# Kernel optimization log

Hardware: AMD Instinct MI355X
Metric: run time of the kernel (lower is better)

## Reference

```python
import jax, jax.numpy as jnp
import numpy as np

NB, NLOC, NALL, NNEI = 1, 4096, 6144, 64
N_EDGE, N_ANGLE, A_SEL = 262144, 409600, 10
N_DIM, E_DIM, A_DIM, AXIS = 128, 64, 32, 4
SEL_REDUCE = 10.0


def _lin_params(key, din, dout):
    k1, k2 = jax.random.split(key)
    W = jax.random.normal(k1, (din, dout), jnp.float32) / np.float32(np.sqrt(din))
    b = jax.random.normal(k2, (dout,), jnp.float32) * 0.01
    return W, b


def setup_inputs():
    key = jax.random.key(0)
    ks = jax.random.split(key, 20)
    inp = {}
    inp["node_ebd_ext"] = jax.random.normal(ks[0], (NB, NALL, N_DIM), jnp.float32)
    inp["edge_ebd"] = jax.random.normal(ks[1], (N_EDGE, E_DIM), jnp.float32)
    inp["h2"] = jax.random.normal(ks[2], (N_EDGE, 3), jnp.float32)
    inp["angle_ebd"] = jax.random.normal(ks[3], (N_ANGLE, A_DIM), jnp.float32)
    inp["nlist"] = jax.random.randint(ks[4], (NB, NLOC, NNEI), 0, NALL)
    inp["nlist_mask"] = jnp.ones((NB, NLOC, NNEI), jnp.bool_)
    inp["sw"] = jax.random.uniform(ks[5], (N_EDGE,), jnp.float32)
    inp["a_nlist"] = jax.random.randint(ks[6], (NB, NLOC, A_SEL), 0, NALL)
    inp["a_nlist_mask"] = jnp.ones((NB, NLOC, A_SEL), jnp.bool_)
    inp["a_sw"] = jax.random.uniform(ks[7], (N_ANGLE,), jnp.float32)
    n2e = jax.random.randint(ks[8], (N_EDGE,), 0, NB * NLOC)
    n_ext2e = jax.random.randint(ks[9], (N_EDGE,), 0, NB * NALL)
    inp["edge_index"] = jnp.stack([n2e, n_ext2e])
    n2a = jax.random.randint(ks[10], (N_ANGLE,), 0, NB * NLOC)
    eij2a = jax.random.randint(ks[11], (N_ANGLE,), 0, N_EDGE)
    eik2a = jax.random.randint(ks[12], (N_ANGLE,), 0, N_EDGE)
    inp["angle_index"] = jnp.stack([n2a, eij2a, eik2a])
    sym_dim = (N_DIM + E_DIM) * AXIS          # 768
    edge_info_dim = 2 * N_DIM + E_DIM         # 320
    angle_dim = A_DIM + N_DIM + 2 * E_DIM     # 288
    inp["W_node_self"], inp["b_node_self"] = _lin_params(ks[13], N_DIM, N_DIM)
    inp["W_node_sym"], inp["b_node_sym"] = _lin_params(ks[14], sym_dim, N_DIM)
    inp["W_node_edge"], inp["b_node_edge"] = _lin_params(ks[15], edge_info_dim, N_DIM)
    inp["W_edge_self"], inp["b_edge_self"] = _lin_params(ks[16], edge_info_dim, E_DIM)
    inp["W_edge_angle1"], inp["b_edge_angle1"] = _lin_params(ks[17], angle_dim, E_DIM)
    inp["W_edge_angle2"], inp["b_edge_angle2"] = _lin_params(ks[18], E_DIM, E_DIM)
    inp["W_angle_self"], inp["b_angle_self"] = _lin_params(ks[19], angle_dim, A_DIM)
    inp["n_res0"] = jnp.full((N_DIM,), 0.1, jnp.float32)
    inp["n_res1"] = jnp.full((N_DIM,), 0.1, jnp.float32)
    inp["n_res2"] = jnp.full((N_DIM,), 0.1, jnp.float32)
    inp["e_res0"] = jnp.full((E_DIM,), 0.1, jnp.float32)
    inp["e_res1"] = jnp.full((E_DIM,), 0.1, jnp.float32)
    inp["a_res0"] = jnp.full((A_DIM,), 0.1, jnp.float32)
    return inp


def reference(node_ebd_ext, edge_ebd, h2, angle_ebd, nlist, nlist_mask, sw,
              a_nlist, a_nlist_mask, a_sw, edge_index, angle_index,
              W_node_self, b_node_self, W_node_sym, b_node_sym,
              W_node_edge, b_node_edge, W_edge_self, b_edge_self,
              W_edge_angle1, b_edge_angle1, W_edge_angle2, b_edge_angle2,
              W_angle_self, b_angle_self,
              n_res0, n_res1, n_res2, e_res0, e_res1, a_res0):
    act = jax.nn.silu
    nb, nloc, nnei = nlist.shape
    n_dim = node_ebd_ext.shape[-1]
    n_edge = h2.shape[0]
    dyn_e_sel = nnei / SEL_REDUCE
    dyn_a_sel = a_nlist.shape[-1] / SEL_REDUCE
    node_ebd = node_ebd_ext[:, :nloc]
    n2e, n_ext2e = edge_index[0], edge_index[1]
    n2a, eij2a, eik2a = angle_index[0], angle_index[1], angle_index[2]
    nei_node_ebd = node_ebd_ext.reshape(-1, n_dim)[n_ext2e]  # [n_edge, n_dim]
    node_self = act(node_ebd @ W_node_self + b_node_self)

    def sym_op(flat_ebd):
        # symmetrization: outer(h2, sw*ebd) scattered to owners, then grrg
        d = flat_ebd.shape[-1]
        w = flat_ebd * sw[:, None]
        h2g2 = jax.ops.segment_sum(
            (h2[:, :, None] * w[:, None, :]).reshape(n_edge, 3 * d),
            n2e, num_segments=nb * nloc)
        h2g2 = h2g2.reshape(nb, nloc, 3, d) * (dyn_e_sel ** -0.5)
        m = h2g2[..., :AXIS]  # [nb, nloc, 3, axis]
        g = jnp.einsum('blxa,blxd->blad', m, h2g2) / 3.0
        return g.reshape(nb, nloc, AXIS * d)

    sym_edge = sym_op(edge_ebd)
    sym_node = sym_op(nei_node_ebd)
    node_sym = act(jnp.concatenate([sym_edge, sym_node], -1) @ W_node_sym + b_node_sym)
    node_i = node_ebd.reshape(-1, n_dim)[n2e]
    edge_info = jnp.concatenate([node_i, nei_node_ebd, edge_ebd], -1)  # [n_edge, 320]
    node_edge_update = act(edge_info @ W_node_edge + b_node_edge) * sw[:, None]
    node_edge_msg = jax.ops.segment_sum(node_edge_update, n2e, num_segments=nb * nloc).reshape(nb, nloc, -1) / dyn_e_sel
    n_updated = node_ebd + n_res0 * node_self + n_res1 * node_sym + n_res2 * node_edge_msg
    edge_self = act(edge_info @ W_edge_self + b_edge_self)
    node_for_angle = node_ebd.reshape(-1, n_dim)[n2a]
    edge_ik = edge_ebd[eik2a]
    edge_ij = edge_ebd[eij2a]
    angle_info = jnp.concatenate([angle_ebd, node_for_angle, edge_ik, edge_ij], -1)  # [n_angle, 288]
    edge_angle = act(angle_info @ W_edge_angle1 + b_edge_angle1)
    reduced = jax.ops.segment_sum(edge_angle * a_sw[:, None], eij2a, num_segments=n_edge) / (dyn_a_sel ** 0.5)
    edge_angle_msg = act(reduced @ W_edge_angle2 + b_edge_angle2)
    e_updated = edge_ebd + e_res0 * edge_self + e_res1 * edge_angle_msg
    angle_self = act(angle_info @ W_angle_self + b_angle_self)
    a_updated = angle_ebd + a_res0 * angle_self
    return (n_updated, e_updated, a_updated)
```

## Files before the change

kernel.cpp:

```cpp
#include <hip/hip_runtime.h>
#include <hip/hip_bf16.h>

#define NLOC_   4096
#define NALL_   6144
#define NEDGE_  262144
#define NANGLE_ 409600

typedef __bf16 bf16x8 __attribute__((ext_vector_type(8)));
typedef float  f32x4  __attribute__((ext_vector_type(4)));
typedef unsigned short u16;

__device__ __forceinline__ float silu_(float x){ return x / (1.0f + __expf(-x)); }

__device__ __forceinline__ u16 f2bu(float f){
    union { float f; unsigned u; } v; v.f = f;
    unsigned r = v.u + 0x7fffu + ((v.u >> 16) & 1u);
    return (u16)(r >> 16);
}
__device__ __forceinline__ float bu2f(u16 b){
    union { unsigned u; float f; } v; v.u = ((unsigned)b) << 16; return v.f;
}
__device__ __forceinline__ void st_bf16x4(u16* dst, float4 v){
    unsigned lo = (unsigned)f2bu(v.x) | ((unsigned)f2bu(v.y) << 16);
    unsigned hi = (unsigned)f2bu(v.z) | ((unsigned)f2bu(v.w) << 16);
    *reinterpret_cast<uint2*>(dst) = make_uint2(lo, hi);
}

__global__ void k_prep(const float* __restrict__ Wne, const float* __restrict__ Wes,
                       const float* __restrict__ W1,  const float* __restrict__ WA,
                       const float* __restrict__ W2,  const float* __restrict__ Wsym,
                       const float* __restrict__ Wns,
                       u16* __restrict__ WTe, u16* __restrict__ WTa, u16* __restrict__ WT2,
                       u16* __restrict__ WsymT, u16* __restrict__ WnsT)
{
    int b = blockIdx.x, t = threadIdx.x;
    if (b < 192) {
        if (t < 320) WTe[b*320 + t] = f2bu(b < 128 ? Wne[t*128 + b] : Wes[t*64 + (b-128)]);
    } else if (b < 288) {
        int n = b - 192;
        if (t < 288) WTa[n*288 + t] = f2bu(n < 64 ? W1[t*64 + n] : WA[t*32 + (n-64)]);
    } else if (b < 352) {
        int n = b - 288;
        if (t < 64)  WT2[n*64 + t] = f2bu(W2[t*64 + n]);
    } else if (b < 480) {
        int n = b - 352;
        if (t < 768) WsymT[n*768 + t] = f2bu(Wsym[t*128 + n]);
    } else {
        int n = b - 480;
        if (t < 128) WnsT[n*128 + t] = f2bu(Wns[t*128 + n]);
    }
}

__global__ void k_cvt(const float* __restrict__ src, u16* __restrict__ dst, int n4)
{
    int i = blockIdx.x * 256 + threadIdx.x;
    int stride = gridDim.x * 256;
    for (; i < n4; i += stride) {
        float4 v = ((const float4*)src)[i];
        st_bf16x4(&dst[(size_t)i*4], v);
    }
}

__global__ __launch_bounds__(256) void k_nconst(
    const u16* __restrict__ NB, const u16* __restrict__ WTe,
    float* __restrict__ nconst)
{
    __shared__ __align__(16) u16 sN[64][136];
    const int tid = threadIdx.x;
    const int e0 = blockIdx.x * 64;
    #pragma unroll
    for (int f = tid; f < 1024; f += 256) {
        int r = f >> 4, c = f & 15;
        *(uint4*)&sN[r][8*c] = ((const uint4*)&NB[(size_t)(e0 + r)*128])[c];
    }
    __syncthreads();

    const int w = tid >> 6, l = tid & 63;
    const int lr = l & 15, hq = l >> 4, lk = hq * 8;

    f32x4 acc[4][3] = {};
    #pragma unroll
    for (int kk = 0; kk < 4; ++kk) {
        bf16x8 a[4], b[3];
        #pragma unroll
        for (int m = 0; m < 4; ++m)
            a[m] = *(const bf16x8*)&sN[16*m + lr][kk*32 + lk];
        #pragma unroll
        for (int nf = 0; nf < 3; ++nf)
            b[nf] = *(const bf16x8*)&WTe[(size_t)(48*w + 16*nf + lr)*320 + kk*32 + lk];
        #pragma unroll
        for (int m = 0; m < 4; ++m)
            #pragma unroll
            for (int nf = 0; nf < 3; ++nf)
                acc[m][nf] = __builtin_amdgcn_mfma_f32_16x16x32_bf16(a[m], b[nf], acc[m][nf], 0, 0, 0);
    }
    #pragma unroll
    for (int nf = 0; nf < 3; ++nf) {
        int c = 48*w + 16*nf + lr;
        #pragma unroll
        for (int m = 0; m < 4; ++m)
            #pragma unroll
            for (int j = 0; j < 4; ++j) {
                int r = 16*m + 4*hq + j;
                nconst[(size_t)(e0 + r)*192 + c] = acc[m][nf][j];
            }
    }
}

__global__ void k_count(const int* __restrict__ key, int* __restrict__ cnt)
{
    int e = blockIdx.x * 256 + threadIdx.x;
    atomicAdd(&cnt[key[e]], 1);
}

__global__ void k_scan(const int* __restrict__ cnt, int* __restrict__ off,
                       int* __restrict__ cursor)
{
    __shared__ int wa[1024];
    int t = threadIdx.x;
    int a0 = cnt[4*t], a1 = cnt[4*t+1], a2 = cnt[4*t+2], a3 = cnt[4*t+3];
    int s1 = a0 + a1, s2 = s1 + a2, s3 = s2 + a3;
    wa[t] = s3;
    __syncthreads();
    for (int d = 1; d < 1024; d <<= 1) {
        int x = wa[t];
        int y = (t >= d) ? wa[t-d] : 0;
        __syncthreads();
        wa[t] = x + y;
        __syncthreads();
    }
    int excl = (t == 0) ? 0 : wa[t-1];
    off[4*t]   = excl;        cursor[4*t]   = excl;
    off[4*t+1] = excl + a0;   cursor[4*t+1] = excl + a0;
    off[4*t+2] = excl + s1;   cursor[4*t+2] = excl + s1;
    off[4*t+3] = excl + s2;   cursor[4*t+3] = excl + s2;
    if (t == 1023) off[4096] = excl + s3;
}

__global__ void k_fill_both(const int* __restrict__ key, int* __restrict__ cursor,
                            int* __restrict__ csr, int* __restrict__ rank)
{
    int e = blockIdx.x * 256 + threadIdx.x;
    int pos = atomicAdd(&cursor[key[e]], 1);
    csr[pos] = e;
    rank[e] = pos;
}

__global__ void k_fill_rank(const int* __restrict__ key, int* __restrict__ cursor,
                            int* __restrict__ rank)
{
    int e = blockIdx.x * 256 + threadIdx.x;
    int pos = atomicAdd(&cursor[key[e]], 1);
    rank[e] = pos;
}

__global__ void k_scan2a(const int* __restrict__ cnt2, int* __restrict__ bsum)
{
    __shared__ int wa[256];
    int b = blockIdx.x, t = threadIdx.x;
    int4 v = ((const int4*)cnt2)[b*256 + t];
    wa[t] = v.x + v.y + v.z + v.w;
    __syncthreads();
    for (int d = 128; d > 0; d >>= 1) {
        if (t < d) wa[t] += wa[t+d];
        __syncthreads();
    }
    if (t == 0) bsum[b] = wa[0];
}

__global__ void k_scan2b(const int* __restrict__ bsum, int* __restrict__ boff)
{
    __shared__ int wa[256];
    int t = threadIdx.x;
    wa[t] = bsum[t];
    __syncthreads();
    for (int d = 1; d < 256; d <<= 1) {
        int x = wa[t];
        int y = (t >= d) ? wa[t-d] : 0;
        __syncthreads();
        wa[t] = x + y;
        __syncthreads();
    }
    boff[t] = (t == 0) ? 0 : wa[t-1];
}

__global__ void k_scan2c(const int* __restrict__ cnt2, const int* __restrict__ boff,
                         int* __restrict__ off2, int* __restrict__ cursor2)
{
    __shared__ int wa[256];
    int b = blockIdx.x, t = threadIdx.x;
    int4 v = ((const int4*)cnt2)[b*256 + t];
    int s1 = v.x, s2 = s1 + v.y, s3 = s2 + v.z, s4 = s3 + v.w;
    wa[t] = s4;
    __syncthreads();
    for (int d = 1; d < 256; d <<= 1) {
        int x = wa[t];
        int y = (t >= d) ? wa[t-d] : 0;
        __syncthreads();
        wa[t] = x + y;
        __syncthreads();
    }
    int base = boff[b] + ((t == 0) ? 0 : wa[t-1]);
    int i = (b*256 + t)*4;
    off2[i]   = base;      cursor2[i]   = base;
    off2[i+1] = base + s1; cursor2[i+1] = base + s1;
    off2[i+2] = base + s2; cursor2[i+2] = base + s2;
    off2[i+3] = base + s3; cursor2[i+3] = base + s3;
    if (b == 255 && t == 255) off2[NEDGE_] = NANGLE_;
}

__global__ __launch_bounds__(256, 4) void k_edge_flat(
    const u16* __restrict__ NB, const u16* __restrict__ EB,
    const float* __restrict__ h2, const float* __restrict__ sw,
    const int* __restrict__ n2e, const int* __restrict__ n_ext2e,
    const int* __restrict__ csr,
    const u16* __restrict__ WTe, const float* __restrict__ nconst,
    const float* __restrict__ bne, const float* __restrict__ bes,
    float* __restrict__ msg,
    float* __restrict__ h2g2_e, float* __restrict__ h2g2_n,
    u16* __restrict__ eselfB)
{
    __shared__ __align__(16) u16 sA[64][200];
    __shared__ float sH[4][576];
    __shared__ int   s_eid[64];
    __shared__ int   s_node[64];
    __shared__ int   s_g[64];
    __shared__ float s_sw[64];
    __shared__ float s_h2[64][3];
    __shared__ int   s_segstart[65];
    __shared__ int   s_nseg;

    const int tid = threadIdx.x;
    const int w  = tid >> 6, l = tid & 63;
    const int lr = l & 15, hq = l >> 4, lk = hq * 8;
    const int base = blockIdx.x * 64;

    if (tid < 64) {
        int e = csr[base + tid];
        s_eid[tid]  = e;
        s_node[tid] = n2e[e];
        s_g[tid]    = n_ext2e[e];
        s_sw[tid]   = sw[e];
        s_h2[tid][0] = h2[e*3];
        s_h2[tid][1] = h2[e*3+1];
        s_h2[tid][2] = h2[e*3+2];
    }
    __syncthreads();

    if (tid < 64) {
        bool flag = (tid == 0) || (s_node[tid] != s_node[tid-1]);
        unsigned long long mask = __ballot(flag);
        if (flag) {
            int sid = __popcll(mask & ((1ull << tid) - 1ull));
            s_segstart[sid] = tid;
        }
        if (tid == 0) {
            int ns = __popcll(mask);
            s_nseg = ns;
            s_segstart[ns] = 64;
        }
    }

    #pragma unroll
    for (int f = tid; f < 1024; f += 256) {
        int r = f >> 4, c = f & 15;
        *(uint4*)&sA[r][8*c] = ((const uint4*)&NB[(size_t)s_g[r]*128])[c];
    }
    #pragma unroll
    for (int f = tid; f < 512; f += 256) {
        int r = f >> 3, c = f & 7;
        *(uint4*)&sA[r][128 + 8*c] = ((const uint4*)&EB[(size_t)s_eid[r]*64])[c];
    }
    __syncthreads();

    float bias[3];
    int   cful[3];
    #pragma unroll
    for (int nf = 0; nf < 3; ++nf) {
        int c = 48*w + 16*nf + lr;
        cful[nf] = c;
        bias[nf] = (c < 128) ? bne[c] : bes[c-128];
    }

    f32x4 acc[4][3] = {};
    #pragma unroll
    for (int kk = 0; kk < 6; ++kk) {
        bf16x8 a[4], b[3];
        #pragma unroll
        for (int m = 0; m < 4; ++m)
            a[m] = *(const bf16x8*)&sA[16*m + lr][kk*32 + lk];
        #pragma unroll
        for (int nf = 0; nf < 3; ++nf)
            b[nf] = *(const bf16x8*)&WTe[(size_t)cful[nf]*320 + 128 + kk*32 + lk];
        #pragma unroll
        for (int m = 0; m < 4; ++m)
            #pragma unroll
            for (int nf = 0; nf < 3; ++nf)
                acc[m][nf] = __builtin_amdgcn_mfma_f32_16x16x32_bf16(a[m], b[nf], acc[m][nf], 0, 0, 0);
    }

    #pragma unroll
    for (int nf = 0; nf < 3; ++nf) {
        int c = cful[nf];
        if (c < 128) {
            #pragma unroll
            for (int m = 0; m < 4; ++m)
                #pragma unroll
                for (int j = 0; j < 4; ++j) {
                    int r = 16*m + 4*hq + j;
                    float ncv = nconst[(size_t)s_node[r]*192 + c];
                    acc[m][nf][j] = silu_(acc[m][nf][j] + ncv + bias[nf]) * s_sw[r];
                }
        } else {
            int c2 = c - 128;
            #pragma unroll
            for (int m = 0; m < 4; ++m)
                #pragma unroll
                for (int j = 0; j < 4; ++j) {
                    int r = 16*m + 4*hq + j;
                    float ncv = nconst[(size_t)s_node[r]*192 + c];
                    eselfB[(size_t)(base + r)*64 + c2] =
                        f2bu(silu_(acc[m][nf][j] + ncv + bias[nf]));
                }
        }
    }

    const int nseg = s_nseg;
    for (int s = 0; s < nseg; ++s) {
        int rs = s_segstart[s], re = s_segstart[s+1];
        int nd = s_node[rs];
        #pragma unroll
        for (int nf = 0; nf < 3; ++nf) {
            if (cful[nf] >= 128) continue;
            float v = 0.f;
            #pragma unroll
            for (int m = 0; m < 4; ++m)
                #pragma unroll
                for (int j = 0; j < 4; ++j) {
                    int r = 16*m + 4*hq + j;
                    v += (r >= rs && r < re) ? acc[m][nf][j] : 0.f;
                }
            v += __shfl_xor(v, 16);
            v += __shfl_xor(v, 32);
            if (hq == 0) atomicAdd(&msg[(size_t)nd*128 + cful[nf]], v);
        }
    }

    for (int s = 0; s < nseg; ++s) {
        int rs = s_segstart[s], re = s_segstart[s+1];
        int nd = s_node[rs];
        int lo = max(16*w, rs), hi = min(16*w + 16, re);
        float hacc[9] = {0.f,0.f,0.f,0.f,0.f,0.f,0.f,0.f,0.f};
        for (int r = lo; r < hi; ++r) {
            float swv = s_sw[r];
            float s0 = s_h2[r][0] * swv;
            float s1 = s_h2[r][1] * swv;
            float s2 = s_h2[r][2] * swv;
            float eb = bu2f(sA[r][128 + l]);
            float n0 = bu2f(sA[r][l]);
            float n1 = bu2f(sA[r][64 + l]);
            hacc[0] = fmaf(s0, eb, hacc[0]);
            hacc[1] = fmaf(s1, eb, hacc[1]);
            hacc[2] = fmaf(s2, eb, hacc[2]);
            hacc[3] = fmaf(s0, n0, hacc[3]);
            hacc[4] = fmaf(s0, n1, hacc[4]);
            hacc[5] = fmaf(s1, n0, hacc[5]);
            hacc[6] = fmaf(s1, n1, hacc[6]);
            hacc[7] = fmaf(s2, n0, hacc[7]);
            hacc[8] = fmaf(s2, n1, hacc[8]);
        }
        #pragma unroll
        for (int q = 0; q < 3; ++q) sH[w][q*64 + l] = hacc[q];
        #pragma unroll
        for (int q = 0; q < 6; ++q) sH[w][192 + q*64 + l] = hacc[3+q];
        __syncthreads();
        for (int i = tid; i < 576; i += 256) {
            float v = sH[0][i] + sH[1][i] + sH[2][i] + sH[3][i];
            if (i < 192) atomicAdd(&h2g2_e[(size_t)nd*192 + i], v);
            else         atomicAdd(&h2g2_n[(size_t)nd*384 + (i - 192)], v);
        }
        __syncthreads();
    }
}

__global__ __launch_bounds__(256) void k_angle_mfma(
    const u16* __restrict__ NB, const u16* __restrict__ EB,
    const u16* __restrict__ AB, const float* __restrict__ a_sw,
    const int* __restrict__ n2a, const int* __restrict__ eij2a,
    const int* __restrict__ eik2a, const int* __restrict__ rank2,
    const u16* __restrict__ WTa,
    const float* __restrict__ b1, const float* __restrict__ bA,
    const float* __restrict__ a_res0,
    u16* __restrict__ ea, float* __restrict__ a_out)
{
    __shared__ __align__(16) u16 sA[32][296];
    __shared__ __align__(16) u16 sEA[32][64];
    __shared__ int s_na[32], s_ij[32], s_ik[32], s_rk[32];
    __shared__ float s_asw[32];
    const int tid = threadIdx.x;
    const int a0 = blockIdx.x * 32;

    if (tid < 32) {
        s_na[tid] = n2a[a0 + tid];
        s_ij[tid] = eij2a[a0 + tid];
        s_ik[tid] = eik2a[a0 + tid];
        s_rk[tid] = rank2[a0 + tid];
        s_asw[tid] = a_sw[a0 + tid];
    }
    __syncthreads();

    if (tid < 128) {
        int r = tid >> 2, c = tid & 3;
        *(uint4*)&sA[r][8*c] = ((const uint4*)&AB[(size_t)(a0 + r)*32])[c];
    }
    #pragma unroll
    for (int f = tid; f < 512; f += 256) {
        int r = f >> 4, c = f & 15;
        *(uint4*)&sA[r][32 + 8*c] = ((const uint4*)&NB[(size_t)s_na[r]*128])[c];
    }
    if (tid < 256) {
        int r = tid >> 3, c = tid & 7;
        *(uint4*)&sA[r][160 + 8*c] = ((const uint4*)&EB[(size_t)s_ik[r]*64])[c];
    }
    {
        int f = tid;
        if (f < 256) {
            int r = f >> 3, c = f & 7;
            *(uint4*)&sA[r][224 + 8*c] = ((const uint4*)&EB[(size_t)s_ij[r]*64])[c];
        }
    }
    __syncthreads();

    const int w = tid >> 6, l = tid & 63;
    const int lr = l & 15, hq = l >> 4, lk = hq * 8;
    const int mrow  = (w & 1) * 16;
    const int nbase = (w >> 1) * 48;

    f32x4 acc[3] = {};
    #pragma unroll
    for (int kk = 0; kk < 9; ++kk) {
        bf16x8 a = *(const bf16x8*)&sA[mrow + lr][kk*32 + lk];
        #pragma unroll
        for (int nf = 0; nf < 3; ++nf) {
            bf16x8 b = *(const bf16x8*)&WTa[(size_t)(nbase + 16*nf + lr)*288 + kk*32 + lk];
            acc[nf] = __builtin_amdgcn_mfma_f32_16x16x32_bf16(a, b, acc[nf], 0, 0, 0);
        }
    }

    #pragma unroll
    for (int nf = 0; nf < 3; ++nf) {
        int c = nbase + 16*nf + lr;
        if (c < 64) {
            float bb = b1[c];
            #pragma unroll
            for (int j = 0; j < 4; ++j) {
                int r = mrow + 4*hq + j;
                sEA[r][c] = f2bu(silu_(acc[nf][j] + bb) * s_asw[r]);
            }
        } else {
            int c2 = c - 64;
            float bb = bA[c2], rr = a_res0[c2];
            #pragma unroll
            for (int j = 0; j < 4; ++j) {
                int r = mrow + 4*hq + j;
                size_t idx = (size_t)(a0 + r)*32 + c2;
                a_out[idx] = bu2f(sA[r][c2]) + rr * silu_(acc[nf][j] + bb);
            }
        }
    }
    __syncthreads();

    if (tid < 256) {
        int r = tid >> 3, c = tid & 7;
        *(uint4*)&ea[(size_t)s_rk[r]*64 + 8*c] = *(const uint4*)&sEA[r][8*c];
    }
}

__global__ __launch_bounds__(256) void k_edgefin_mfma(
    const u16* __restrict__ EB, const u16* __restrict__ eselfB,
    const int* __restrict__ rank_e,
    const u16* __restrict__ ea, const int* __restrict__ off2,
    const u16* __restrict__ WT2,
    const float* __restrict__ b2_, const float* __restrict__ er0,
    const float* __restrict__ er1,
    float* __restrict__ e_out)
{
    __shared__ __align__(16) u16 sR[64][72];
    __shared__ __align__(16) u16 sE[64][72];
    __shared__ __align__(16) u16 sB[64][72];
    __shared__ int s_rk[64];
    const int tid = threadIdx.x;
    const int e0 = blockIdx.x * 64;
    const int w = tid >> 6, l = tid & 63;

    if (tid < 64) s_rk[tid] = rank_e[e0 + tid];
    __syncthreads();

    #pragma unroll
    for (int f = tid; f < 512; f += 256) {
        int r = f >> 3, c = f & 7;
        *(uint4*)&sB[r][8*c] = ((const uint4*)&EB[(size_t)(e0 + r)*64])[c];
        *(uint4*)&sE[r][8*c] = ((const uint4*)&eselfB[(size_t)s_rk[r]*64])[c];
    }

    #pragma unroll
    for (int r16 = 0; r16 < 16; ++r16) {
        int r = w*16 + r16;
        int e = e0 + r;
        float s = 0.f;
        int jb = off2[e], je = off2[e+1];
        for (int j = jb; j < je; ++j)
            s += bu2f(ea[(size_t)j*64 + l]);
        sR[r][l] = f2bu(s);
    }
    __syncthreads();

    const int lr = l & 15, hq = l >> 4, lk = hq * 8;

    f32x4 acc[4] = {};
    #pragma unroll
    for (int kk = 0; kk < 2; ++kk) {
        bf16x8 b = *(const bf16x8*)&WT2[(size_t)(16*w + lr)*64 + kk*32 + lk];
        #pragma unroll
        for (int m = 0; m < 4; ++m) {
            bf16x8 a = *(const bf16x8*)&sR[16*m + lr][kk*32 + lk];
            acc[m] = __builtin_amdgcn_mfma_f32_16x16x32_bf16(a, b, acc[m], 0, 0, 0);
        }
    }
    int c = 16*w + lr;
    float bb = b2_[c], r0 = er0[c], r1 = er1[c];
    #pragma unroll
    for (int m = 0; m < 4; ++m)
        #pragma unroll
        for (int j = 0; j < 4; ++j) {
            int r = 16*m + 4*hq + j;
            size_t idx = (size_t)(e0 + r)*64 + c;
            e_out[idx] = bu2f(sB[r][c]) + r0 * bu2f(sE[r][c])
                       + r1 * silu_(acc[m][j] + bb);
        }
}

__global__ void k_symc(const float* __restrict__ h2g2_e,
                       const float* __restrict__ h2g2_n,
                       u16* __restrict__ symcB)
{
    __shared__ float he[192];
    __shared__ float hn[384];
    int n = blockIdx.x;
    int t = threadIdx.x;
    for (int i = t; i < 192; i += 128) he[i] = h2g2_e[(size_t)n*192 + i];
    for (int i = t; i < 384; i += 128) hn[i] = h2g2_n[(size_t)n*384 + i];
    __syncthreads();
    const float SCALE = 1.0f / (6.4f * 3.0f);
    for (int i = t; i < 768; i += 128) {
        float s;
        if (i < 256) {
            int a = i >> 6, j = i & 63;
            s = he[a]*he[j] + he[64+a]*he[64+j] + he[128+a]*he[128+j];
        } else {
            int i2 = i - 256;
            int a = i2 >> 7, j = i2 & 127;
            s = hn[a]*hn[j] + hn[128+a]*hn[128+j] + hn[256+a]*hn[256+j];
        }
        symcB[(size_t)n*768 + i] = f2bu(s * SCALE);
    }
}

__global__ __launch_bounds__(256) void k_node_mfma(
    const u16* __restrict__ symcB, const u16* __restrict__ NB,
    const float* __restrict__ node_ext, const float* __restrict__ msg,
    const u16* __restrict__ WsymT, const u16* __restrict__ WnsT,
    const float* __restrict__ bns, const float* __restrict__ bsym,
    const float* __restrict__ nr0, const float* __restrict__ nr1,
    const float* __restrict__ nr2,
    float* __restrict__ n_out)
{
    __shared__ __align__(16) u16 sA[32][264];
    const int tid = threadIdx.x;
    const int n0 = blockIdx.x * 32;
    const int w = tid >> 6, l = tid & 63;
    const int lr = l & 15, hq = l >> 4, lk = hq * 8;

    f32x4 accY[2][2] = {};
    f32x4 accS[2][2] = {};

    for (int chunk = 0; chunk < 3; ++chunk) {
        __syncthreads();
        #pragma unroll
        for (int f = tid; f < 1024; f += 256) {
            int r = f >> 5, c = f & 31;
            *(uint4*)&sA[r][8*c] =
                ((const uint4*)&symcB[(size_t)(n0 + r)*768 + chunk*256])[c];
        }
        __syncthreads();
        #pragma unroll
        for (int kk = 0; kk < 8; ++kk) {
            bf16x8 a[2], b[2];
            #pragma unroll
            for (int m = 0; m < 2; ++m)
                a[m] = *(const bf16x8*)&sA[16*m + lr][kk*32 + lk];
            #pragma unroll
            for (int nf = 0; nf < 2; ++nf)
                b[nf] = *(const bf16x8*)&WsymT[(size_t)(32*w + 16*nf + lr)*768
                                               + chunk*256 + kk*32 + lk];
            #pragma unroll
            for (int m = 0; m < 2; ++m)
                #pragma unroll
                for (int nf = 0; nf < 2; ++nf)
                    accY[m][nf] = __builtin_amdgcn_mfma_f32_16x16x32_bf16(a[m], b[nf], accY[m][nf], 0, 0, 0);
        }
    }

    __syncthreads();
    #pragma unroll
    for (int f = tid; f < 512; f += 256) {
        int r = f >> 4, c = f & 15;
        *(uint4*)&sA[r][8*c] = ((const uint4*)&NB[(size_t)(n0 + r)*128])[c];
    }
    __syncthreads();
    #pragma unroll
    for (int kk = 0; kk < 4; ++kk) {
        bf16x8 a[2], b[2];
        #pragma unroll
        for (int m = 0; m < 2; ++m)
            a[m] = *(const bf16x8*)&sA[16*m + lr][kk*32 + lk];
        #pragma unroll
        for (int nf = 0; nf < 2; ++nf)
            b[nf] = *(const bf16x8*)&WnsT[(size_t)(32*w + 16*nf + lr)*128 + kk*32 + lk];
        #pragma unroll
        for (int m = 0; m < 2; ++m)
            #pragma unroll
            for (int nf = 0; nf < 2; ++nf)
                accS[m][nf] = __builtin_amdgcn_mfma_f32_16x16x32_bf16(a[m], b[nf], accS[m][nf], 0, 0, 0);
    }

    #pragma unroll
    for (int nf = 0; nf < 2; ++nf) {
        int c = 32*w + 16*nf + lr;
        float bS = bns[c], bY = bsym[c];
        float r0 = nr0[c], r1 = nr1[c], r2 = nr2[c];
        #pragma unroll
        for (int m = 0; m < 2; ++m)
            #pragma unroll
            for (int j = 0; j < 4; ++j) {
                int r = 16*m + 4*hq + j;
                size_t idx = (size_t)(n0 + r)*128 + c;
                float self_ = silu_(accS[m][nf][j] + bS);
                float sym_  = silu_(accY[m][nf][j] + bY);
                n_out[idx] = node_ext[idx] + r0*self_ + r1*sym_
                           + r2 * msg[idx] * (1.0f / 6.4f);
            }
    }
}

extern "C" void kernel_launch(void* const* d_in, const int* in_sizes, int n_in,
                              void* d_out, int out_size, void* d_ws, size_t ws_size,
                              hipStream_t stream)
{
    const float* node_ext  = (const float*)d_in[0];
    const float* edge_ebd  = (const float*)d_in[1];
    const float* h2        = (const float*)d_in[2];
    const float* angle_ebd = (const float*)d_in[3];
    const float* sw        = (const float*)d_in[6];
    const float* a_sw      = (const float*)d_in[9];
    const int*  edge_index  = (const int*)d_in[10];
    const int*  angle_index = (const int*)d_in[11];
    const int* n2e     = edge_index;
    const int* n_ext2e = edge_index + NEDGE_;
    const int* n2a     = angle_index;
    const int* eij2a   = angle_index + NANGLE_;
    const int* eik2a   = angle_index + 2*NANGLE_;

    const float* Wns  = (const float*)d_in[12];
    const float* bns  = (const float*)d_in[13];
    const float* Wsym = (const float*)d_in[14];
    const float* bsym = (const float*)d_in[15];
    const float* Wne  = (const float*)d_in[16];
    const float* bne  = (const float*)d_in[17];
    const float* Wes  = (const float*)d_in[18];
    const float* bes  = (const float*)d_in[19];
    const float* W1   = (const float*)d_in[20];
    const float* b1   = (const float*)d_in[21];
    const float* W2   = (const float*)d_in[22];
    const float* b2_  = (const float*)d_in[23];
    const float* WA   = (const float*)d_in[24];
    const float* bA   = (const float*)d_in[25];
    const float* nr0  = (const float*)d_in[26];
    const float* nr1  = (const float*)d_in[27];
    const float* nr2  = (const float*)d_in[28];
    const float* er0  = (const float*)d_in[29];
    const float* er1  = (const float*)d_in[30];
    const float* ar0  = (const float*)d_in[31];

    char* wsp = (char*)d_ws;
    u16*   ea      = (u16*)wsp;    wsp += (size_t)NANGLE_ * 64 * 2;
    u16*   EB      = (u16*)wsp;    wsp += (size_t)NEDGE_ * 64 * 2;
    u16*   NB      = (u16*)wsp;    wsp += (size_t)NALL_ * 128 * 2;
    u16*   AB      = (u16*)wsp;    wsp += (size_t)NANGLE_ * 32 * 2;
    u16*   eselfB  = (u16*)wsp;    wsp += (size_t)NEDGE_ * 64 * 2;
    u16*   symcB   = (u16*)wsp;    wsp += (size_t)NLOC_ * 768 * 2;
    int*   cnt     = (int*)wsp;    wsp += 4096 * 4;
    int*   cnt2    = (int*)wsp;    wsp += (size_t)NEDGE_ * 4;
    float* msg     = (float*)wsp;  wsp += (size_t)NLOC_ * 128 * 4;
    float* h2g2_e  = (float*)wsp;  wsp += (size_t)NLOC_ * 192 * 4;
    float* h2g2_n  = (float*)wsp;  wsp += (size_t)NLOC_ * 384 * 4;
    size_t zero_bytes = 4096*4 + (size_t)NEDGE_*4 + (size_t)NLOC_*128*4
                      + (size_t)NLOC_*192*4 + (size_t)NLOC_*384*4;
    int*   off     = (int*)wsp;    wsp += 4104 * 4;
    int*   cursor  = (int*)wsp;    wsp += 4096 * 4;
    int*   csr     = (int*)wsp;    wsp += (size_t)NEDGE_ * 4;
    int*   rank_e  = (int*)wsp;    wsp += (size_t)NEDGE_ * 4;
    int*   off2    = (int*)wsp;    wsp += ((size_t)NEDGE_ + 16) * 4;
    int*   cursor2 = (int*)wsp;    wsp += (size_t)NEDGE_ * 4;
    int*   bsum    = (int*)wsp;    wsp += 256 * 4;
    int*   boff    = (int*)wsp;    wsp += 256 * 4;
    int*   rank2   = (int*)wsp;    wsp += (size_t)NANGLE_ * 4;
    float* nconst  = (float*)wsp;  wsp += (size_t)NLOC_ * 192 * 4;
    u16*   WTe     = (u16*)wsp;    wsp += 192 * 320 * 2;
    u16*   WTa     = (u16*)wsp;    wsp += 96 * 288 * 2;
    u16*   WT2     = (u16*)wsp;    wsp += 64 * 64 * 2;
    u16*   WsymT   = (u16*)wsp;    wsp += 128 * 768 * 2;
    u16*   WnsT    = (u16*)wsp;    wsp += 128 * 128 * 2;

    hipMemsetAsync(cnt, 0, zero_bytes, stream);

    float* n_out = (float*)d_out;
    float* e_out = n_out + (size_t)NLOC_ * 128;
    float* a_out = e_out + (size_t)NEDGE_ * 64;

    k_prep   <<<608, 768, 0, stream>>>(Wne, Wes, W1, WA, W2, Wsym, Wns,
                                       WTe, WTa, WT2, WsymT, WnsT);
    k_cvt    <<<768, 256, 0, stream>>>(node_ext, NB, NALL_*128/4);
    k_cvt    <<<4096, 256, 0, stream>>>(edge_ebd, EB, NEDGE_*64/4);
    k_cvt    <<<4096, 256, 0, stream>>>(angle_ebd, AB, NANGLE_*32/4);
    k_count  <<<NEDGE_/256, 256, 0, stream>>>(n2e, cnt);
    k_scan   <<<1, 1024, 0, stream>>>(cnt, off, cursor);
    k_fill_both <<<NEDGE_/256, 256, 0, stream>>>(n2e, cursor, csr, rank_e);
    k_count  <<<NANGLE_/256, 256, 0, stream>>>(eij2a, cnt2);
    k_scan2a <<<256, 256, 0, stream>>>(cnt2, bsum);
    k_scan2b <<<1, 256, 0, stream>>>(bsum, boff);
    k_scan2c <<<256, 256, 0, stream>>>(cnt2, boff, off2, cursor2);
    k_fill_rank <<<NANGLE_/256, 256, 0, stream>>>(eij2a, cursor2, rank2);

    k_nconst <<<NLOC_/64, 256, 0, stream>>>(NB, WTe, nconst);
    k_edge_flat <<<NEDGE_/64, 256, 0, stream>>>(NB, EB, h2, sw, n2e, n_ext2e, csr,
                                                WTe, nconst, bne, bes,
                                                msg, h2g2_e, h2g2_n, eselfB);
    k_angle_mfma <<<NANGLE_/32, 256, 0, stream>>>(NB, EB, AB, a_sw,
                                                  n2a, eij2a, eik2a, rank2,
                                                  WTa, b1, bA, ar0, ea, a_out);
    k_edgefin_mfma <<<NEDGE_/64, 256, 0, stream>>>(EB, eselfB, rank_e, ea, off2,
                                                   WT2, b2_, er0, er1, e_out);
    k_symc   <<<NLOC_, 128, 0, stream>>>(h2g2_e, h2g2_n, symcB);
    k_node_mfma <<<NLOC_/32, 256, 0, stream>>>(symcB, NB, node_ext, msg,
                                               WsymT, WnsT, bns, bsym,
                                               nr0, nr1, nr2, n_out);
}
```

Before: 454.3 us.

## Merge prep, scan, fill and finish kernels into fewer launches; drop rank_e

The weight transposes, bf16 conversions and both histogram counts move into one multi-role kernel. The first scan, the block sums and nconst share a second launch, and the two CSR fills run in a third. Edge-self outputs are now written at the original edge id instead of the sorted rank, which removes the rank_e array and its indirection in the finish kernel. The symc work is folded into the finish kernel. This cuts launch count and serialization, but it is heterogeneous block dispatch with possible imbalance. Writing eselfO by original edge id makes those stores scattered.

```diff
diff --git a/kernel.cpp b/kernel.cpp
--- a/kernel.cpp
+++ b/kernel.cpp
@@ -26,146 +26,139 @@
     *reinterpret_cast<uint2*>(dst) = make_uint2(lo, hi);
 }
 
-__global__ void k_prep(const float* __restrict__ Wne, const float* __restrict__ Wes,
-                       const float* __restrict__ W1,  const float* __restrict__ WA,
-                       const float* __restrict__ W2,  const float* __restrict__ Wsym,
-                       const float* __restrict__ Wns,
-                       u16* __restrict__ WTe, u16* __restrict__ WTa, u16* __restrict__ WT2,
-                       u16* __restrict__ WsymT, u16* __restrict__ WnsT)
-{
-    int b = blockIdx.x, t = threadIdx.x;
-    if (b < 192) {
-        if (t < 320) WTe[b*320 + t] = f2bu(b < 128 ? Wne[t*128 + b] : Wes[t*64 + (b-128)]);
-    } else if (b < 288) {
-        int n = b - 192;
-        if (t < 288) WTa[n*288 + t] = f2bu(n < 64 ? W1[t*64 + n] : WA[t*32 + (n-64)]);
-    } else if (b < 352) {
-        int n = b - 288;
-        if (t < 64)  WT2[n*64 + t] = f2bu(W2[t*64 + n]);
-    } else if (b < 480) {
-        int n = b - 352;
-        if (t < 768) WsymT[n*768 + t] = f2bu(Wsym[t*128 + n]);
+__global__ __launch_bounds__(256) void k_mega_prep(
+    const float* __restrict__ Wne, const float* __restrict__ Wes,
+    const float* __restrict__ W1,  const float* __restrict__ WA,
+    const float* __restrict__ W2,  const float* __restrict__ Wsym,
+    const float* __restrict__ Wns,
+    const float* __restrict__ node_ext, const float* __restrict__ edge_ebd,
+    const float* __restrict__ angle_ebd,
+    const int* __restrict__ n2e, const int* __restrict__ eij2a,
+    u16* __restrict__ WTe, u16* __restrict__ WTa, u16* __restrict__ WT2,
+    u16* __restrict__ WsymT, u16* __restrict__ WnsT,
+    u16* __restrict__ NB, u16* __restrict__ EB, u16* __restrict__ AB,
+    int* __restrict__ cnt, int* __restrict__ cnt2)
+{
+    const int b = blockIdx.x, tid = threadIdx.x;
+    if (b < 812) {
+        int i = b*256 + tid;
+        if (i < 61440) {
+            int r = i/320, c = i - r*320;
+            WTe[i] = f2bu(r < 128 ? Wne[c*128 + r] : Wes[c*64 + (r-128)]);
+        } else if (i < 89088) {
+            int j = i - 61440; int r = j/288, c = j - r*288;
+            WTa[j] = f2bu(r < 64 ? W1[c*64 + r] : WA[c*32 + (r-64)]);
+        } else if (i < 93184) {
+            int j = i - 89088; int r = j >> 6, c = j & 63;
+            WT2[j] = f2bu(W2[c*64 + r]);
+        } else if (i < 191488) {
+            int j = i - 93184; int r = j/768, c = j - r*768;
+            WsymT[j] = f2bu(Wsym[c*128 + r]);
+        } else {
+            int j = i - 191488; int r = j >> 7, c = j & 127;
+            WnsT[j] = f2bu(Wns[c*128 + r]);
+        }
+    } else if (b < 1580) {
+        int i = (b - 812)*256 + tid;
+        float4 v = ((const float4*)node_ext)[i];
+        st_bf16x4(&NB[(size_t)i*4], v);
+    } else if (b < 3628) {
+        for (int i = (b - 1580)*256 + tid; i < NEDGE_*64/4; i += 2048*256) {
+            float4 v = ((const float4*)edge_ebd)[i];
+            st_bf16x4(&EB[(size_t)i*4], v);
+        }
+    } else if (b < 5676) {
+        for (int i = (b - 3628)*256 + tid; i < NANGLE_*32/4; i += 2048*256) {
+            float4 v = ((const float4*)angle_ebd)[i];
+            st_bf16x4(&AB[(size_t)i*4], v);
+        }
+    } else if (b < 6700) {
+        int e = (b - 5676)*256 + tid;
+        atomicAdd(&cnt[n2e[e]], 1);
     } else {
-        int n = b - 480;
-        if (t < 128) WnsT[n*128 + t] = f2bu(Wns[t*128 + n]);
-    }
-}
-
-__global__ void k_cvt(const float* __restrict__ src, u16* __restrict__ dst, int n4)
-{
-    int i = blockIdx.x * 256 + threadIdx.x;
-    int stride = gridDim.x * 256;
-    for (; i < n4; i += stride) {
-        float4 v = ((const float4*)src)[i];
-        st_bf16x4(&dst[(size_t)i*4], v);
-    }
-}
-
-__global__ __launch_bounds__(256) void k_nconst(
+        int a = (b - 6700)*256 + tid;
+        atomicAdd(&cnt2[eij2a[a]], 1);
+    }
+}
+
+__global__ __launch_bounds__(256) void k_scan_misc(
+    const int* __restrict__ cnt, int* __restrict__ off, int* __restrict__ cursor,
+    const int* __restrict__ cnt2, int* __restrict__ bsum,
     const u16* __restrict__ NB, const u16* __restrict__ WTe,
     float* __restrict__ nconst)
 {
     __shared__ __align__(16) u16 sN[64][136];
-    const int tid = threadIdx.x;
-    const int e0 = blockIdx.x * 64;
-    #pragma unroll
-    for (int f = tid; f < 1024; f += 256) {
-        int r = f >> 4, c = f & 15;
-        *(uint4*)&sN[r][8*c] = ((const uint4*)&NB[(size_t)(e0 + r)*128])[c];
-    }
-    __syncthreads();
-
-    const int w = tid >> 6, l = tid & 63;
-    const int lr = l & 15, hq = l >> 4, lk = hq * 8;
-
-    f32x4 acc[4][3] = {};
-    #pragma unroll
-    for (int kk = 0; kk < 4; ++kk) {
-        bf16x8 a[4], b[3];
-        #pragma unroll
-        for (int m = 0; m < 4; ++m)
-            a[m] = *(const bf16x8*)&sN[16*m + lr][kk*32 + lk];
-        #pragma unroll
-        for (int nf = 0; nf < 3; ++nf)
-            b[nf] = *(const bf16x8*)&WTe[(size_t)(48*w + 16*nf + lr)*320 + kk*32 + lk];
-        #pragma unroll
-        for (int m = 0; m < 4; ++m)
+    int* wa = (int*)&sN[0][0];
+    const int b = blockIdx.x, t = threadIdx.x;
+
+    if (b == 0) {
+        int v[16]; int s = 0;
+        #pragma unroll
+        for (int k = 0; k < 16; ++k) { v[k] = s; s += cnt[16*t + k]; }
+        wa[t] = s;
+        __syncthreads();
+        for (int d = 1; d < 256; d <<= 1) {
+            int x = wa[t];
+            int y = (t >= d) ? wa[t-d] : 0;
+            __syncthreads();
+            wa[t] = x + y;
+            __syncthreads();
+        }
+        int excl = (t == 0) ? 0 : wa[t-1];
+        #pragma unroll
+        for (int k = 0; k < 16; ++k) {
+            off[16*t + k]    = excl + v[k];
+            cursor[16*t + k] = excl + v[k];
+        }
+        if (t == 255) off[4096] = excl + s;
+    } else if (b <= 256) {
+        int bb = b - 1;
+        int4 v = ((const int4*)cnt2)[bb*256 + t];
+        wa[t] = v.x + v.y + v.z + v.w;
+        __syncthreads();
+        for (int d = 128; d > 0; d >>= 1) {
+            if (t < d) wa[t] += wa[t+d];
+            __syncthreads();
+        }
+        if (t == 0) bsum[bb] = wa[0];
+    } else {
+        const int e0 = (b - 257) * 64;
+        #pragma unroll
+        for (int f = t; f < 1024; f += 256) {
+            int r = f >> 4, c = f & 15;
+            *(uint4*)&sN[r][8*c] = ((const uint4*)&NB[(size_t)(e0 + r)*128])[c];
+        }
+        __syncthreads();
+        const int w = t >> 6, l = t & 63;
+        const int lr = l & 15, hq = l >> 4, lk = hq * 8;
+        f32x4 acc[4][3] = {};
+        #pragma unroll
+        for (int kk = 0; kk < 4; ++kk) {
+            bf16x8 a[4], bb[3];
+            #pragma unroll
+            for (int m = 0; m < 4; ++m)
+                a[m] = *(const bf16x8*)&sN[16*m + lr][kk*32 + lk];
             #pragma unroll
             for (int nf = 0; nf < 3; ++nf)
-                acc[m][nf] = __builtin_amdgcn_mfma_f32_16x16x32_bf16(a[m], b[nf], acc[m][nf], 0, 0, 0);
-    }
-    #pragma unroll
-    for (int nf = 0; nf < 3; ++nf) {
-        int c = 48*w + 16*nf + lr;
-        #pragma unroll
-        for (int m = 0; m < 4; ++m)
-            #pragma unroll
-            for (int j = 0; j < 4; ++j) {
-                int r = 16*m + 4*hq + j;
-                nconst[(size_t)(e0 + r)*192 + c] = acc[m][nf][j];
-            }
-    }
-}
-
-__global__ void k_count(const int* __restrict__ key, int* __restrict__ cnt)
-{
-    int e = blockIdx.x * 256 + threadIdx.x;
-    atomicAdd(&cnt[key[e]], 1);
-}
-
-__global__ void k_scan(const int* __restrict__ cnt, int* __restrict__ off,
-                       int* __restrict__ cursor)
-{
-    __shared__ int wa[1024];
-    int t = threadIdx.x;
-    int a0 = cnt[4*t], a1 = cnt[4*t+1], a2 = cnt[4*t+2], a3 = cnt[4*t+3];
-    int s1 = a0 + a1, s2 = s1 + a2, s3 = s2 + a3;
-    wa[t] = s3;
-    __syncthreads();
-    for (int d = 1; d < 1024; d <<= 1) {
-        int x = wa[t];
-        int y = (t >= d) ? wa[t-d] : 0;
-        __syncthreads();
-        wa[t] = x + y;
-        __syncthreads();
-    }
-    int excl = (t == 0) ? 0 : wa[t-1];
-    off[4*t]   = excl;        cursor[4*t]   = excl;
-    off[4*t+1] = excl + a0;   cursor[4*t+1] = excl + a0;
-    off[4*t+2] = excl + s1;   cursor[4*t+2] = excl + s1;
-    off[4*t+3] = excl + s2;   cursor[4*t+3] = excl + s2;
-    if (t == 1023) off[4096] = excl + s3;
-}
-
-__global__ void k_fill_both(const int* __restrict__ key, int* __restrict__ cursor,
-                            int* __restrict__ csr, int* __restrict__ rank)
-{
-    int e = blockIdx.x * 256 + threadIdx.x;
-    int pos = atomicAdd(&cursor[key[e]], 1);
-    csr[pos] = e;
-    rank[e] = pos;
-}
-
-__global__ void k_fill_rank(const int* __restrict__ key, int* __restrict__ cursor,
-                            int* __restrict__ rank)
-{
-    int e = blockIdx.x * 256 + threadIdx.x;
-    int pos = atomicAdd(&cursor[key[e]], 1);
-    rank[e] = pos;
-}
-
-__global__ void k_scan2a(const int* __restrict__ cnt2, int* __restrict__ bsum)
-{
-    __shared__ int wa[256];
-    int b = blockIdx.x, t = threadIdx.x;
-    int4 v = ((const int4*)cnt2)[b*256 + t];
-    wa[t] = v.x + v.y + v.z + v.w;
-    __syncthreads();
-    for (int d = 128; d > 0; d >>= 1) {
-        if (t < d) wa[t] += wa[t+d];
-        __syncthreads();
-    }
-    if (t == 0) bsum[b] = wa[0];
+                bb[nf] = *(const bf16x8*)&WTe[(size_t)(48*w + 16*nf + lr)*320 + kk*32 + lk];
+            #pragma unroll
+            for (int m = 0; m < 4; ++m)
+                #pragma unroll
+                for (int nf = 0; nf < 3; ++nf)
+                    acc[m][nf] = __builtin_amdgcn_mfma_f32_16x16x32_bf16(a[m], bb[nf], acc[m][nf], 0, 0, 0);
+        }
+        #pragma unroll
+        for (int nf = 0; nf < 3; ++nf) {
+            int c = 48*w + 16*nf + lr;
+            #pragma unroll
+            for (int m = 0; m < 4; ++m)
+                #pragma unroll
+                for (int j = 0; j < 4; ++j) {
+                    int r = 16*m + 4*hq + j;
+                    nconst[(size_t)(e0 + r)*192 + c] = acc[m][nf][j];
+                }
+        }
+    }
 }
 
 __global__ void k_scan2b(const int* __restrict__ bsum, int* __restrict__ boff)
@@ -207,6 +200,23 @@
     off2[i+2] = base + s2; cursor2[i+2] = base + s2;
     off2[i+3] = base + s3; cursor2[i+3] = base + s3;
     if (b == 255 && t == 255) off2[NEDGE_] = NANGLE_;
+}
+
+__global__ void k_fill2(const int* __restrict__ n2e, int* __restrict__ cursor,
+                        int* __restrict__ csr,
+                        const int* __restrict__ eij2a, int* __restrict__ cursor2,
+                        int* __restrict__ rank2)
+{
+    int b = blockIdx.x;
+    if (b < 1024) {
+        int e = b*256 + threadIdx.x;
+        int pos = atomicAdd(&cursor[n2e[e]], 1);
+        csr[pos] = e;
+    } else {
+        int a = (b - 1024)*256 + threadIdx.x;
+        int pos = atomicAdd(&cursor2[eij2a[a]], 1);
+        rank2[a] = pos;
+    }
 }
 
 __global__ __launch_bounds__(256, 4) void k_edge_flat(
@@ -218,7 +228,7 @@
     const float* __restrict__ bne, const float* __restrict__ bes,
     float* __restrict__ msg,
     float* __restrict__ h2g2_e, float* __restrict__ h2g2_n,
-    u16* __restrict__ eselfB)
+    u16* __restrict__ eselfO)
 {
     __shared__ __align__(16) u16 sA[64][200];
     __shared__ float sH[4][576];
@@ -319,7 +329,7 @@
                 for (int j = 0; j < 4; ++j) {
                     int r = 16*m + 4*hq + j;
                     float ncv = nconst[(size_t)s_node[r]*192 + c];
-                    eselfB[(size_t)(base + r)*64 + c2] =
+                    eselfO[(size_t)s_eid[r]*64 + c2] =
                         f2bu(silu_(acc[m][nf][j] + ncv + bias[nf]));
                 }
         }
@@ -418,16 +428,10 @@
         int r = f >> 4, c = f & 15;
         *(uint4*)&sA[r][32 + 8*c] = ((const uint4*)&NB[(size_t)s_na[r]*128])[c];
     }
-    if (tid < 256) {
+    {
         int r = tid >> 3, c = tid & 7;
         *(uint4*)&sA[r][160 + 8*c] = ((const uint4*)&EB[(size_t)s_ik[r]*64])[c];
-    }
-    {
-        int f = tid;
-        if (f < 256) {
-            int r = f >> 3, c = f & 7;
-            *(uint4*)&sA[r][224 + 8*c] = ((const uint4*)&EB[(size_t)s_ij[r]*64])[c];
-        }
+        *(uint4*)&sA[r][224 + 8*c] = ((const uint4*)&EB[(size_t)s_ij[r]*64])[c];
     }
     __syncthreads();
 
@@ -470,99 +474,93 @@
     }
     __syncthreads();
 
-    if (tid < 256) {
+    {
         int r = tid >> 3, c = tid & 7;
         *(uint4*)&ea[(size_t)s_rk[r]*64 + 8*c] = *(const uint4*)&sEA[r][8*c];
     }
 }
 
-__global__ __launch_bounds__(256) void k_edgefin_mfma(
-    const u16* __restrict__ EB, const u16* __restrict__ eselfB,
-    const int* __restrict__ rank_e,
+__global__ __launch_bounds__(256) void k_fin(
+    const u16* __restrict__ EB, const u16* __restrict__ eselfO,
     const u16* __restrict__ ea, const int* __restrict__ off2,
     const u16* __restrict__ WT2,
     const float* __restrict__ b2_, const float* __restrict__ er0,
     const float* __restrict__ er1,
-    float* __restrict__ e_out)
+    float* __restrict__ e_out,
+    const float* __restrict__ h2g2_e, const float* __restrict__ h2g2_n,
+    u16* __restrict__ symcB)
 {
     __shared__ __align__(16) u16 sR[64][72];
     __shared__ __align__(16) u16 sE[64][72];
     __shared__ __align__(16) u16 sB[64][72];
-    __shared__ int s_rk[64];
     const int tid = threadIdx.x;
-    const int e0 = blockIdx.x * 64;
-    const int w = tid >> 6, l = tid & 63;
-
-    if (tid < 64) s_rk[tid] = rank_e[e0 + tid];
-    __syncthreads();
-
-    #pragma unroll
-    for (int f = tid; f < 512; f += 256) {
-        int r = f >> 3, c = f & 7;
-        *(uint4*)&sB[r][8*c] = ((const uint4*)&EB[(size_t)(e0 + r)*64])[c];
-        *(uint4*)&sE[r][8*c] = ((const uint4*)&eselfB[(size_t)s_rk[r]*64])[c];
-    }
-
-    #pragma unroll
-    for (int r16 = 0; r16 < 16; ++r16) {
-        int r = w*16 + r16;
-        int e = e0 + r;
-        float s = 0.f;
-        int jb = off2[e], je = off2[e+1];
-        for (int j = jb; j < je; ++j)
-            s += bu2f(ea[(size_t)j*64 + l]);
-        sR[r][l] = f2bu(s);
-    }
-    __syncthreads();
-
-    const int lr = l & 15, hq = l >> 4, lk = hq * 8;
-
-    f32x4 acc[4] = {};
-    #pragma unroll
-    for (int kk = 0; kk < 2; ++kk) {
-        bf16x8 b = *(const bf16x8*)&WT2[(size_t)(16*w + lr)*64 + kk*32 + lk];
-        #pragma unroll
-        for (int m = 0; m < 4; ++m) {
-            bf16x8 a = *(const bf16x8*)&sR[16*m + lr][kk*32 + lk];
-            acc[m] = __builtin_amdgcn_mfma_f32_16x16x32_bf16(a, b, acc[m], 0, 0, 0);
-        }
-    }
-    int c = 16*w + lr;
-    float bb = b2_[c], r0 = er0[c], r1 = er1[c];
-    #pragma unroll
-    for (int m = 0; m < 4; ++m)
-        #pragma unroll
-        for (int j = 0; j < 4; ++j) {
-            int r = 16*m + 4*hq + j;
-            size_t idx = (size_t)(e0 + r)*64 + c;
-            e_out[idx] = bu2f(sB[r][c]) + r0 * bu2f(sE[r][c])
-                       + r1 * silu_(acc[m][j] + bb);
-        }
-}
-
-__global__ void k_symc(const float* __restrict__ h2g2_e,
-                       const float* __restrict__ h2g2_n,
-                       u16* __restrict__ symcB)
-{
-    __shared__ float he[192];
-    __shared__ float hn[384];
-    int n = blockIdx.x;
-    int t = threadIdx.x;
-    for (int i = t; i < 192; i += 128) he[i] = h2g2_e[(size_t)n*192 + i];
-    for (int i = t; i < 384; i += 128) hn[i] = h2g2_n[(size_t)n*384 + i];
-    __syncthreads();
-    const float SCALE = 1.0f / (6.4f * 3.0f);
-    for (int i = t; i < 768; i += 128) {
-        float s;
-        if (i < 256) {
-            int a = i >> 6, j = i & 63;
-            s = he[a]*he[j] + he[64+a]*he[64+j] + he[128+a]*he[128+j];
-        } else {
-            int i2 = i - 256;
-            int a = i2 >> 7, j = i2 & 127;
-            s = hn[a]*hn[j] + hn[128+a]*hn[128+j] + hn[256+a]*hn[256+j];
-        }
-        symcB[(size_t)n*768 + i] = f2bu(s * SCALE);
+    const int blk = blockIdx.x;
+
+    if (blk < 4096) {
+        const int e0 = blk * 64;
+        const int w = tid >> 6, l = tid & 63;
+
+        #pragma unroll
+        for (int f = tid; f < 512; f += 256) {
+            int r = f >> 3, c = f & 7;
+            *(uint4*)&sB[r][8*c] = ((const uint4*)&EB[(size_t)(e0 + r)*64])[c];
+            *(uint4*)&sE[r][8*c] = ((const uint4*)&eselfO[(size_t)(e0 + r)*64])[c];
+        }
+
+        #pragma unroll
+        for (int r16 = 0; r16 < 16; ++r16) {
+            int r = w*16 + r16;
+            int e = e0 + r;
+            float s = 0.f;
+            int jb = off2[e], je = off2[e+1];
+            for (int j = jb; j < je; ++j)
+                s += bu2f(ea[(size_t)j*64 + l]);
+            sR[r][l] = f2bu(s);
+        }
+        __syncthreads();
+
+        const int lr = l & 15, hq = l >> 4, lk = hq * 8;
+        f32x4 acc[4] = {};
+        #pragma unroll
+        for (int kk = 0; kk < 2; ++kk) {
+            bf16x8 b = *(const bf16x8*)&WT2[(size_t)(16*w + lr)*64 + kk*32 + lk];
+            #pragma unroll
+            for (int m = 0; m < 4; ++m) {
+                bf16x8 a = *(const bf16x8*)&sR[16*m + lr][kk*32 + lk];
+                acc[m] = __builtin_amdgcn_mfma_f32_16x16x32_bf16(a, b, acc[m], 0, 0, 0);
+            }
+        }
+        int c = 16*w + lr;
+        float bb = b2_[c], r0 = er0[c], r1 = er1[c];
+        #pragma unroll
+        for (int m = 0; m < 4; ++m)
+            #pragma unroll
+            for (int j = 0; j < 4; ++j) {
+                int r = 16*m + 4*hq + j;
+                size_t idx = (size_t)(e0 + r)*64 + c;
+                e_out[idx] = bu2f(sB[r][c]) + r0 * bu2f(sE[r][c])
+                           + r1 * silu_(acc[m][j] + bb);
+            }
+    } else {
+        const int n = blk - 4096;
+        float* he = (float*)&sR[0][0];
+        float* hn = he + 192;
+        for (int i = tid; i < 192; i += 256) he[i] = h2g2_e[(size_t)n*192 + i];
+        for (int i = tid; i < 384; i += 256) hn[i] = h2g2_n[(size_t)n*384 + i];
+        __syncthreads();
+        const float SCALE = 1.0f / (6.4f * 3.0f);
+        for (int i = tid; i < 768; i += 256) {
+            float s;
+            if (i < 256) {
+                int a = i >> 6, j = i & 63;
+                s = he[a]*he[j] + he[64+a]*he[64+j] + he[128+a]*he[128+j];
+            } else {
+                int i2 = i - 256;
+                int a = i2 >> 7, j = i2 & 127;
+                s = hn[a]*hn[j] + hn[128+a]*hn[128+j] + hn[256+a]*hn[256+j];
+            }
+            symcB[(size_t)n*768 + i] = f2bu(s * SCALE);
+        }
     }
 }
 
@@ -697,7 +695,7 @@
     u16*   EB      = (u16*)wsp;    wsp += (size_t)NEDGE_ * 64 * 2;
     u16*   NB      = (u16*)wsp;    wsp += (size_t)NALL_ * 128 * 2;
     u16*   AB      = (u16*)wsp;    wsp += (size_t)NANGLE_ * 32 * 2;
-    u16*   eselfB  = (u16*)wsp;    wsp += (size_t)NEDGE_ * 64 * 2;
+    u16*   eselfO  = (u16*)wsp;    wsp += (size_t)NEDGE_ * 64 * 2;
     u16*   symcB   = (u16*)wsp;    wsp += (size_t)NLOC_ * 768 * 2;
     int*   cnt     = (int*)wsp;    wsp += 4096 * 4;
     int*   cnt2    = (int*)wsp;    wsp += (size_t)NEDGE_ * 4;
@@ -709,7 +707,6 @@
     int*   off     = (int*)wsp;    wsp += 4104 * 4;
     int*   cursor  = (int*)wsp;    wsp += 4096 * 4;
     int*   csr     = (int*)wsp;    wsp += (size_t)NEDGE_ * 4;
-    int*   rank_e  = (int*)wsp;    wsp += (size_t)NEDGE_ * 4;
     int*   off2    = (int*)wsp;    wsp += ((size_t)NEDGE_ + 16) * 4;
     int*   cursor2 = (int*)wsp;    wsp += (size_t)NEDGE_ * 4;
     int*   bsum    = (int*)wsp;    wsp += 256 * 4;
@@ -728,30 +725,25 @@
     float* e_out = n_out + (size_t)NLOC_ * 128;
     float* a_out = e_out + (size_t)NEDGE_ * 64;
 
-    k_prep   <<<608, 768, 0, stream>>>(Wne, Wes, W1, WA, W2, Wsym, Wns,
-                                       WTe, WTa, WT2, WsymT, WnsT);
-    k_cvt    <<<768, 256, 0, stream>>>(node_ext, NB, NALL_*128/4);
-    k_cvt    <<<4096, 256, 0, stream>>>(edge_ebd, EB, NEDGE_*64/4);
-    k_cvt    <<<4096, 256, 0, stream>>>(angle_ebd, AB, NANGLE_*32/4);
-    k_count  <<<NEDGE_/256, 256, 0, stream>>>(n2e, cnt);
-    k_scan   <<<1, 1024, 0, stream>>>(cnt, off, cursor);
-    k_fill_both <<<NEDGE_/256, 256, 0, stream>>>(n2e, cursor, csr, rank_e);
-    k_count  <<<NANGLE_/256, 256, 0, stream>>>(eij2a, cnt2);
-    k_scan2a <<<256, 256, 0, stream>>>(cnt2, bsum);
+    k_mega_prep <<<8300, 256, 0, stream>>>(Wne, Wes, W1, WA, W2, Wsym, Wns,
+                                           node_ext, edge_ebd, angle_ebd,
+                                           n2e, eij2a,
+                                           WTe, WTa, WT2, WsymT, WnsT,
+                                           NB, EB, AB, cnt, cnt2);
+    k_scan_misc <<<321, 256, 0, stream>>>(cnt, off, cursor, cnt2, bsum,
+                                          NB, WTe, nconst);
     k_scan2b <<<1, 256, 0, stream>>>(bsum, boff);
     k_scan2c <<<256, 256, 0, stream>>>(cnt2, boff, off2, cursor2);
-    k_fill_rank <<<NANGLE_/256, 256, 0, stream>>>(eij2a, cursor2, rank2);
-
-    k_nconst <<<NLOC_/64, 256, 0, stream>>>(NB, WTe, nconst);
+    k_fill2  <<<2624, 256, 0, stream>>>(n2e, cursor, csr, eij2a, cursor2, rank2);
+
     k_edge_flat <<<NEDGE_/64, 256, 0, stream>>>(NB, EB, h2, sw, n2e, n_ext2e, csr,
                                                 WTe, nconst, bne, bes,
-                                                msg, h2g2_e, h2g2_n, eselfB);
+                                                msg, h2g2_e, h2g2_n, eselfO);
     k_angle_mfma <<<NANGLE_/32, 256, 0, stream>>>(NB, EB, AB, a_sw,
                                                   n2a, eij2a, eik2a, rank2,
                                                   WTa, b1, bA, ar0, ea, a_out);
-    k_edgefin_mfma <<<NEDGE_/64, 256, 0, stream>>>(EB, eselfB, rank_e, ea, off2,
-                                                   WT2, b2_, er0, er1, e_out);
-    k_symc   <<<NLOC_, 128, 0, stream>>>(h2g2_e, h2g2_n, symcB);
+    k_fin <<<8192, 256, 0, stream>>>(EB, eselfO, ea, off2, WT2, b2_, er0, er1,
+                                     e_out, h2g2_e, h2g2_n, symcB);
     k_node_mfma <<<NLOC_/32, 256, 0, stream>>>(symcB, NB, node_ext, msg,
                                                WsymT, WnsT, bns, bsym,
                                                nr0, nr1, nr2, n_out);
```

Result: faster. 423.8 us (-6.7%).
